# Optimization experiments

Measured on AMD Instinct MI355X. Metric: run time of the kernel, lower is better.

## Reference

```python
import jax, jax.numpy as jnp
import numpy as np
from jax import lax

WINDOW = (3, 7, 7)   # per-axis neighborhood kernel size (odd -> centered window)
TILE = (4, 8, 8)     # query tile per axis (must divide T,H,W); FNA-style tiling


def _axis_window(X, k, tq):
    # NATTEN non-causal, stride=1, dilation=1: query i attends keys [s, s+k)
    # with s = clip(i - (k-1)//2, 0, X-k) (centered, clamped at borders).
    starts = np.clip(np.arange(X) - (k - 1) // 2, 0, X - k)          # [X]
    span = tq + k - 1                                                # key block extent per tile
    lead = np.arange(X // tq) * tq                                   # first query of each tile
    base = np.minimum(starts[lead], X - span)                        # [nt] block start (in-bounds)
    gq = lead[:, None] + np.arange(tq)                                # [nt, tq] global query idx
    s = starts[gq][..., None]                                        # [nt, tq, 1]
    j = base[:, None, None] + np.arange(span)                         # [nt, 1, span] global key idx
    valid = (j >= s) & (j < s + k)                                    # [nt, tq, span]
    return base.astype(np.int32), valid


def _na3d(q, k, v, T, H, W):
    B, L, nh, D = q.shape
    assert L == T * H * W
    kT, kH, kW = WINDOW
    qt, qh, qw = TILE
    assert T % qt == 0 and H % qh == 0 and W % qw == 0
    st, sh, sw = qt + kT - 1, qh + kH - 1, qw + kW - 1
    ntT, ntH, ntW = T // qt, H // qh, W // qw
    N = ntT * ntH * ntW
    qvol, svol = qt * qh * qw, st * sh * sw

    baseT, mT = _axis_window(T, kT, qt)
    baseH, mH = _axis_window(H, kH, qh)
    baseW, mW = _axis_window(W, kW, qw)

    # combined per-tile mask: [N, qvol, svol] (static, small)
    mask = (mT[:, None, None, :, None, None, :, None, None]
            & mH[None, :, None, None, :, None, None, :, None]
            & mW[None, None, :, None, None, :, None, None, :])
    mask = jnp.asarray(mask.reshape(N, qvol, svol))

    bT, bH, bW = np.meshgrid(baseT, baseH, baseW, indexing='ij')
    bT = jnp.asarray(bT.ravel()); bH = jnp.asarray(bH.ravel()); bW = jnp.asarray(bW.ravel())

    def to_grid(x):
        return x.reshape(B, T, H, W, nh, D)
    qg, kg, vg = to_grid(q), to_grid(k), to_grid(v)

    # query tiles -> [N, B, qvol, nh, D]
    qt_ = qg.reshape(B, ntT, qt, ntH, qh, ntW, qw, nh, D)
    qt_ = qt_.transpose(1, 3, 5, 0, 2, 4, 6, 7, 8).reshape(N, B, qvol, nh, D)

    # key/value halo blocks per tile -> [N, B, svol, nh, D]
    def slice_blk(arr, t0, h0, w0):
        return lax.dynamic_slice(arr, (0, t0, h0, w0, 0, 0), (B, st, sh, sw, nh, D))
    kblk = jax.vmap(slice_blk, in_axes=(None, 0, 0, 0))(kg, bT, bH, bW).reshape(N, B, svol, nh, D)
    vblk = jax.vmap(slice_blk, in_axes=(None, 0, 0, 0))(vg, bT, bH, bW).reshape(N, B, svol, nh, D)

    scale = D ** -0.5
    scores = jnp.einsum('nbqhd,nbkhd->nbhqk', qt_, kblk) * scale
    scores = jnp.where(mask[:, None, None], scores, -jnp.inf)
    attn = jax.nn.softmax(scores, axis=-1)
    out = jnp.einsum('nbhqk,nbkhd->nbhqd', attn, vblk)

    # scatter tiles back to [B, L, nh, D]
    out = out.reshape(ntT, ntH, ntW, B, nh, qt, qh, qw, D)
    out = out.transpose(3, 0, 5, 1, 6, 2, 7, 4, 8).reshape(B, L, nh, D)
    return out


def setup_inputs() -> dict:
    key = jax.random.key(0)
    k1, k2, k3 = jax.random.split(key, 3)
    B, nh, D = 1, 8, 128
    T, H, W = 16, 32, 32
    L = T * H * W
    q = jax.random.normal(k1, (B, L, nh, D), jnp.float32)
    kk = jax.random.normal(k2, (B, L, nh, D), jnp.float32)
    v = jax.random.normal(k3, (B, L, nh, D), jnp.float32)
    return {"q": q, "k": kk, "v": v, "video_t": T, "video_h": H, "video_w": W}


def reference(q, k, v, video_t, video_h, video_w):
    return _na3d(q, k, v, video_t, video_h, video_w)
```

## Files before the change

### kernel.cpp

```cpp
#include <hip/hip_runtime.h>


typedef _Float16 f16;
typedef _Float16 half8 __attribute__((ext_vector_type(8)));
typedef _Float16 half4 __attribute__((ext_vector_type(4)));
typedef _Float16 half2 __attribute__((ext_vector_type(2)));
typedef float floatx4 __attribute__((ext_vector_type(4)));
typedef float floatv4 __attribute__((ext_vector_type(4)));

#define CFENCE() asm volatile("" ::: "memory")
#define BAR_PLAIN() do { CFENCE(); __builtin_amdgcn_s_barrier(); CFENCE(); } while (0)
#define BAR_LDSW() do { asm volatile("s_waitcnt lgkmcnt(0)" ::: "memory"); \
                        __builtin_amdgcn_s_barrier(); CFENCE(); } while (0)
#define LIVE_FENCE() do { CFENCE(); __builtin_amdgcn_sched_barrier(0); } while (0)

namespace {

constexpr int T = 16, H = 32, W = 32, NH = 8, D = 128;
constexpr int QT = 2, QH = 4, QW = 8;
constexpr float SCALE = 0.088388347648318447f;

__device__ __forceinline__ int SLOT(int tile, int lr) {
  return tile * 69 + (lr >> 4) * 17 + (lr & 15);
}

__device__ __forceinline__ size_t goff(int tt, int hh, int ww, int head) {
  return ((size_t)((tt * H + hh) * W + ww) * NH + head) * D;
}

__device__ __forceinline__ int div14(int x) { return (x * 586) >> 13; }

__global__ __launch_bounds__(256, 3) void na3d_mfma(
    const float* __restrict__ qp, const float* __restrict__ kp,
    const float* __restrict__ vp, float* __restrict__ op) {
  __shared__ alignas(16) f16 kvbuf[24 * 69 * 8];
  __shared__ alignas(16) f16 pbuf[12 * 69 * 8];

  int bid = (int)(((blockIdx.x & 7) << 8) | (blockIdx.x >> 3));
  const int wb = bid & 3;  bid >>= 2;
  const int hb = bid & 7;  bid >>= 3;
  const int tb = bid & 7;  bid >>= 3;
  const int head = bid;

  const int t0 = tb * QT;
  const int h0 = hb * QH, w0 = wb * QW;
  const int bT = min(max(t0 - 1, 0), T - 4);
  const int bH = min(max(h0 - 3, 0), H - 10);
  const int bW = min(max(w0 - 3, 0), W - 14);

  const int tid = threadIdx.x;
  const int wave = tid >> 6, lane = tid & 63;
  const int quad = lane >> 4, ln = lane & 15;
  const int kbase = quad * 4;

  const int toff = wave >> 1;
  const int hoff = (wave & 1) * 2 + (ln >> 3);
  const int woff = ln & 7;
  const int aT = min(max(t0 + toff - 1, 0), T - 3) - bT;
  const int aH = min(max(h0 + hoff - 3, 0), H - 7) - bH;
  const int aW = min(max(w0 + woff - 3, 0), W - 7) - bW;

  half8 qreg[4];
  {
    const size_t row = goff(t0 + toff, h0 + hoff, w0 + woff, head);
#pragma unroll
    for (int ks = 0; ks < 4; ++ks) {
      const int d0 = ks * 32 + quad * 8;
      const floatv4 x0 = *(const floatv4*)(qp + row + d0);
      const floatv4 x1 = *(const floatv4*)(qp + row + d0 + 4);
      half8 hv;
      hv[0] = (f16)(x0[0] * SCALE); hv[1] = (f16)(x0[1] * SCALE);
      hv[2] = (f16)(x0[2] * SCALE); hv[3] = (f16)(x0[3] * SCALE);
      hv[4] = (f16)(x1[0] * SCALE); hv[5] = (f16)(x1[1] * SCALE);
      hv[6] = (f16)(x1[2] * SCALE); hv[7] = (f16)(x1[3] * SCALE);
      qreg[ks] = hv;
    }
  }

  if (quad >= 2) {
    *(floatx4*)&pbuf[SLOT(wave * 3 + 2, lane) * 8] = (floatx4){0.f, 0.f, 0.f, 0.f};
  }

  floatx4 oacc[8] = {{0.f, 0.f, 0.f, 0.f}, {0.f, 0.f, 0.f, 0.f},
                     {0.f, 0.f, 0.f, 0.f}, {0.f, 0.f, 0.f, 0.f},
                     {0.f, 0.f, 0.f, 0.f}, {0.f, 0.f, 0.f, 0.f},
                     {0.f, 0.f, 0.f, 0.f}, {0.f, 0.f, 0.f, 0.f}};
  float m_run = -1e30f, l_run = 0.f;

  floatv4 kreg[5][2];
  floatv4 vreg[3][4];

  {
    const int tt = bT, kh0 = bH;
#pragma unroll
    for (int it = 0; it < 5; ++it) {
      const int s = tid + it * 256;
      if (s < 1120) {
        const int kk = s >> 4, dg = s & 15;
        const int khl = div14(kk), kw = kk - khl * 14;
        const size_t off = goff(tt, kh0 + khl, bW + kw, head) + dg * 8;
        kreg[it][0] = *(const floatv4*)(kp + off);
        kreg[it][1] = *(const floatv4*)(kp + off + 4);
      }
    }
  }

  for (int c = 0; c < 8; ++c) {
    const int dt = c >> 1;
    const int tt = bT + dt;
    const int kh0 = bH + (c & 1) * 5;
    const int hh5 = (c & 1) * 5;
    const bool tOK = (dt >= aT) && (dt < aT + 3);

    BAR_PLAIN();

#pragma unroll
    for (int it = 0; it < 5; ++it) {
      const int s = tid + it * 256;
      if (s < 1120) {
        const int kk = s >> 4, dg = s & 15;
        const floatv4 a0 = kreg[it][0], a1 = kreg[it][1];
        half8 hv;
        hv[0] = (f16)a0[0]; hv[1] = (f16)a0[1];
        hv[2] = (f16)a0[2]; hv[3] = (f16)a0[3];
        hv[4] = (f16)a1[0]; hv[5] = (f16)a1[1];
        hv[6] = (f16)a1[2]; hv[7] = (f16)a1[3];
        *(half8*)&kvbuf[SLOT((kk >> 4) * 4 + (dg >> 2),
                             (dg & 3) * 16 + (kk & 15)) * 8] = hv;
      }
    }
    LIVE_FENCE();

#pragma unroll
    for (int it = 0; it < 3; ++it) {
      const int s = tid + it * 256;
      const int p = s >> 4, dg = s & 15;
      const int kk0 = p * 2;
      if (kk0 < 70) {
        const int khl = div14(kk0), kw = kk0 - khl * 14;
        const size_t off = goff(tt, kh0 + khl, bW + kw, head) + dg * 8;
        vreg[it][0] = *(const floatv4*)(vp + off);
        vreg[it][1] = *(const floatv4*)(vp + off + 4);
        vreg[it][2] = *(const floatv4*)(vp + off + 1024);
        vreg[it][3] = *(const floatv4*)(vp + off + 1028);
      } else {
        vreg[it][0] = (floatv4){0.f, 0.f, 0.f, 0.f};
        vreg[it][1] = (floatv4){0.f, 0.f, 0.f, 0.f};
        vreg[it][2] = (floatv4){0.f, 0.f, 0.f, 0.f};
        vreg[it][3] = (floatv4){0.f, 0.f, 0.f, 0.f};
      }
    }

    BAR_LDSW();

    floatx4 acc1[5] = {{0.f, 0.f, 0.f, 0.f}, {0.f, 0.f, 0.f, 0.f},
                       {0.f, 0.f, 0.f, 0.f}, {0.f, 0.f, 0.f, 0.f},
                       {0.f, 0.f, 0.f, 0.f}};
    __builtin_amdgcn_s_setprio(1);
#pragma unroll
    for (int kt = 0; kt < 5; ++kt) {
#pragma unroll
      for (int ks = 0; ks < 4; ++ks) {
        const half8 a = *(const half8*)&kvbuf[SLOT(kt * 4 + ks, lane) * 8];
        acc1[kt] =
            __builtin_amdgcn_mfma_f32_16x16x32_f16(a, qreg[ks], acc1[kt], 0, 0, 0);
      }
    }
    __builtin_amdgcn_s_setprio(0);

    BAR_PLAIN();

#pragma unroll
    for (int it = 0; it < 3; ++it) {
      const int s = tid + it * 256;
      const int p = s >> 4, dg = s & 15;
      const int kk0 = p * 2;
      const int kst = kk0 >> 5, qd = (kk0 >> 3) & 3, j0 = kk0 & 7;
      const int tbase = (dg >> 1) * 3 + kst;
      const int lrb = qd * 16 + (dg & 1) * 8;
#pragma unroll
      for (int u = 0; u < 8; ++u) {
        half2 h;
        h[0] = (f16)vreg[it][u >> 2][u & 3];
        h[1] = (f16)vreg[it][2 + (u >> 2)][u & 3];
        *(half2*)&kvbuf[SLOT(tbase, lrb + u) * 8 + j0] = h;
      }
    }
    LIVE_FENCE();

    if (c < 7) {
      const int cc = c + 1;
      const int ttn = bT + (cc >> 1);
      const int kh0n = bH + (cc & 1) * 5;
#pragma unroll
      for (int it = 0; it < 5; ++it) {
        const int s = tid + it * 256;
        if (s < 1120) {
          const int kk = s >> 4, dg = s & 15;
          const int khl = div14(kk), kw = kk - khl * 14;
          const size_t off = goff(ttn, kh0n + khl, bW + kw, head) + dg * 8;
          kreg[it][0] = *(const floatv4*)(kp + off);
          kreg[it][1] = *(const floatv4*)(kp + off + 4);
        }
      }
    }

    float pm = -1e30f;
#pragma unroll
    for (int kt = 0; kt < 5; ++kt) {
#pragma unroll
      for (int r = 0; r < 4; ++r) {
        const int kk = kt * 16 + kbase + r;
        const int khl = div14(kk), kw = kk - khl * 14;
        const int kha = hh5 + khl;
        const bool ok = tOK && (kk < 70) && ((unsigned)(kha - aH) < 7u) &&
                        ((unsigned)(kw - aW) < 7u);
        const float sv = ok ? acc1[kt][r] : -INFINITY;
        acc1[kt][r] = sv;
        pm = fmaxf(pm, sv);
      }
    }
    pm = fmaxf(pm, __shfl_xor(pm, 16));
    pm = fmaxf(pm, __shfl_xor(pm, 32));
    const float mN = fmaxf(m_run, pm);
    const float alpha = __expf(m_run - mN);
    m_run = mN;

    float ps = 0.f;
#pragma unroll
    for (int kt = 0; kt < 5; ++kt) {
      half4 h;
#pragma unroll
      for (int r = 0; r < 4; ++r) {
        const float e = __expf(acc1[kt][r] - mN);
        ps += e;
        h[r] = (f16)e;
      }
      *(half4*)&pbuf[SLOT(wave * 3 + (kt >> 1),
                          ((kt & 1) * 2 + (quad >> 1)) * 16 + ln) * 8 +
                     (quad & 1) * 4] = h;
    }
    ps += __shfl_xor(ps, 16);
    ps += __shfl_xor(ps, 32);
    l_run = l_run * alpha + ps;

    BAR_LDSW();
    __builtin_amdgcn_sched_barrier(0);

    floatx4 af;
#pragma unroll
    for (int r = 0; r < 4; ++r) af[r] = __shfl(alpha, kbase + r);
#pragma unroll
    for (int u = 0; u < 8; ++u) oacc[u] *= af;
    __builtin_amdgcn_s_setprio(1);
#pragma unroll
    for (int ks = 0; ks < 3; ++ks) {
      const half8 a = *(const half8*)&pbuf[SLOT(wave * 3 + ks, lane) * 8];
#pragma unroll
      for (int u = 0; u < 8; ++u) {
        const half8 b = *(const half8*)&kvbuf[SLOT(u * 3 + ks, lane) * 8];
        oacc[u] = __builtin_amdgcn_mfma_f32_16x16x32_f16(a, b, oacc[u], 0, 0, 0);
      }
    }
    __builtin_amdgcn_s_setprio(0);
  }

  const float linv = 1.f / l_run;
  floatx4 lf;
#pragma unroll
  for (int r = 0; r < 4; ++r) lf[r] = __shfl(linv, kbase + r);
#pragma unroll
  for (int r = 0; r < 4; ++r) {
    const int q = wave * 16 + quad * 4 + r;
    const size_t off =
        goff(t0 + (q >> 5), h0 + ((q >> 3) & 3), w0 + (q & 7), head);
#pragma unroll
    for (int u = 0; u < 8; ++u)
      op[off + u * 16 + ln] = oacc[u][r] * lf[r];
  }
}

}

extern "C" void kernel_launch(void* const* d_in, const int* in_sizes, int n_in,
                              void* d_out, int out_size, void* d_ws,
                              size_t ws_size, hipStream_t stream) {
  const float* q = (const float*)d_in[0];
  const float* k = (const float*)d_in[1];
  const float* v = (const float*)d_in[2];
  float* out = (float*)d_out;
  const int nblocks = NH * (T / QT) * (H / QH) * (W / QW);
  na3d_mfma<<<dim3(nblocks), dim3(256), 0, stream>>>(q, k, v, out);
}
```

Before: 456.6 us.

## Split V prefetch to cut register pressure and raise occupancy to four blocks

The third V prefetch group is now loaded after the QK MFMA phase instead of before it, so fewer V registers are live during the score computation. The launch bound is raised from 3 to 4 blocks per SM to take advantage of the lower register pressure. The trade-off is that the delayed V load has less time to hide its global memory latency before it is converted into LDS.

New measurement: 686.7 us. +50.4%, slower.

```diff
diff --git a/kernel.cpp b/kernel.cpp
--- a/kernel.cpp
+++ b/kernel.cpp
@@ -30,7 +30,7 @@
 
 __device__ __forceinline__ int div14(int x) { return (x * 586) >> 13; }
 
-__global__ __launch_bounds__(256, 3) void na3d_mfma(
+__global__ __launch_bounds__(256, 4) void na3d_mfma(
     const float* __restrict__ qp, const float* __restrict__ kp,
     const float* __restrict__ vp, float* __restrict__ op) {
   __shared__ alignas(16) f16 kvbuf[24 * 69 * 8];
@@ -88,7 +88,8 @@
   float m_run = -1e30f, l_run = 0.f;
 
   floatv4 kreg[5][2];
-  floatv4 vreg[3][4];
+  floatv4 vregA[2][4];
+  floatv4 vregB[4];
 
   {
     const int tt = bT, kh0 = bH;
@@ -132,46 +133,58 @@
     LIVE_FENCE();
 
 #pragma unroll
-    for (int it = 0; it < 3; ++it) {
+    for (int it = 0; it < 2; ++it) {
       const int s = tid + it * 256;
+      const int p = s >> 4, dg = s & 15;
+      const int kk0 = p * 2;
+      const int khl = div14(kk0), kw = kk0 - khl * 14;
+      const size_t off = goff(tt, kh0 + khl, bW + kw, head) + dg * 8;
+      vregA[it][0] = *(const floatv4*)(vp + off);
+      vregA[it][1] = *(const floatv4*)(vp + off + 4);
+      vregA[it][2] = *(const floatv4*)(vp + off + 1024);
+      vregA[it][3] = *(const floatv4*)(vp + off + 1028);
+    }
+
+    BAR_LDSW();
+
+    floatx4 acc1[5] = {{0.f, 0.f, 0.f, 0.f}, {0.f, 0.f, 0.f, 0.f},
+                       {0.f, 0.f, 0.f, 0.f}, {0.f, 0.f, 0.f, 0.f},
+                       {0.f, 0.f, 0.f, 0.f}};
+    __builtin_amdgcn_s_setprio(1);
+#pragma unroll
+    for (int kt = 0; kt < 5; ++kt) {
+#pragma unroll
+      for (int ks = 0; ks < 4; ++ks) {
+        const half8 a = *(const half8*)&kvbuf[SLOT(kt * 4 + ks, lane) * 8];
+        acc1[kt] =
+            __builtin_amdgcn_mfma_f32_16x16x32_f16(a, qreg[ks], acc1[kt], 0, 0, 0);
+      }
+    }
+    __builtin_amdgcn_s_setprio(0);
+
+    BAR_PLAIN();
+
+    {
+      const int s = tid + 512;
       const int p = s >> 4, dg = s & 15;
       const int kk0 = p * 2;
       if (kk0 < 70) {
         const int khl = div14(kk0), kw = kk0 - khl * 14;
         const size_t off = goff(tt, kh0 + khl, bW + kw, head) + dg * 8;
-        vreg[it][0] = *(const floatv4*)(vp + off);
-        vreg[it][1] = *(const floatv4*)(vp + off + 4);
-        vreg[it][2] = *(const floatv4*)(vp + off + 1024);
-        vreg[it][3] = *(const floatv4*)(vp + off + 1028);
+        vregB[0] = *(const floatv4*)(vp + off);
+        vregB[1] = *(const floatv4*)(vp + off + 4);
+        vregB[2] = *(const floatv4*)(vp + off + 1024);
+        vregB[3] = *(const floatv4*)(vp + off + 1028);
       } else {
-        vreg[it][0] = (floatv4){0.f, 0.f, 0.f, 0.f};
-        vreg[it][1] = (floatv4){0.f, 0.f, 0.f, 0.f};
-        vreg[it][2] = (floatv4){0.f, 0.f, 0.f, 0.f};
-        vreg[it][3] = (floatv4){0.f, 0.f, 0.f, 0.f};
-      }
-    }
-
-    BAR_LDSW();
-
-    floatx4 acc1[5] = {{0.f, 0.f, 0.f, 0.f}, {0.f, 0.f, 0.f, 0.f},
-                       {0.f, 0.f, 0.f, 0.f}, {0.f, 0.f, 0.f, 0.f},
-                       {0.f, 0.f, 0.f, 0.f}};
-    __builtin_amdgcn_s_setprio(1);
-#pragma unroll
-    for (int kt = 0; kt < 5; ++kt) {
-#pragma unroll
-      for (int ks = 0; ks < 4; ++ks) {
-        const half8 a = *(const half8*)&kvbuf[SLOT(kt * 4 + ks, lane) * 8];
-        acc1[kt] =
-            __builtin_amdgcn_mfma_f32_16x16x32_f16(a, qreg[ks], acc1[kt], 0, 0, 0);
-      }
-    }
-    __builtin_amdgcn_s_setprio(0);
-
-    BAR_PLAIN();
-
-#pragma unroll
-    for (int it = 0; it < 3; ++it) {
+        vregB[0] = (floatv4){0.f, 0.f, 0.f, 0.f};
+        vregB[1] = (floatv4){0.f, 0.f, 0.f, 0.f};
+        vregB[2] = (floatv4){0.f, 0.f, 0.f, 0.f};
+        vregB[3] = (floatv4){0.f, 0.f, 0.f, 0.f};
+      }
+    }
+
+#pragma unroll
+    for (int it = 0; it < 2; ++it) {
       const int s = tid + it * 256;
       const int p = s >> 4, dg = s & 15;
       const int kk0 = p * 2;
@@ -181,8 +194,23 @@
 #pragma unroll
       for (int u = 0; u < 8; ++u) {
         half2 h;
-        h[0] = (f16)vreg[it][u >> 2][u & 3];
-        h[1] = (f16)vreg[it][2 + (u >> 2)][u & 3];
+        h[0] = (f16)vregA[it][u >> 2][u & 3];
+        h[1] = (f16)vregA[it][2 + (u >> 2)][u & 3];
+        *(half2*)&kvbuf[SLOT(tbase, lrb + u) * 8 + j0] = h;
+      }
+    }
+    {
+      const int s = tid + 512;
+      const int p = s >> 4, dg = s & 15;
+      const int kk0 = p * 2;
+      const int kst = kk0 >> 5, qd = (kk0 >> 3) & 3, j0 = kk0 & 7;
+      const int tbase = (dg >> 1) * 3 + kst;
+      const int lrb = qd * 16 + (dg & 1) * 8;
+#pragma unroll
+      for (int u = 0; u < 8; ++u) {
+        half2 h;
+        h[0] = (f16)vregB[u >> 2][u & 3];
+        h[1] = (f16)vregB[2 + (u >> 2)][u & 3];
         *(half2*)&kvbuf[SLOT(tbase, lrb + u) * 8 + j0] = h;
       }
     }
```
